# Optimization experiments

Hardware: AMD Instinct MI355X
Metric: run time of the kernel (lower is better)

Reference implementation:

```python
import jax, jax.numpy as jnp
import numpy as np

EMBED_DIM = 1024
HEAD_NUM = 16
HEAD_DIM = EMBED_DIM // HEAD_NUM
T, B, S = 2048, 4, 2048


def setup_inputs() -> dict:
    key = jax.random.key(0)
    ks = jax.random.split(key, 11)
    s = 0.02
    return {
        "query": jax.random.normal(ks[0], (T, B, EMBED_DIM), jnp.float32),
        "key": jax.random.normal(ks[1], (S, B, EMBED_DIM), jnp.float32),
        "value": jax.random.normal(ks[2], (S, B, EMBED_DIM), jnp.float32),
        "q_proj_weight": jax.random.normal(ks[3], (EMBED_DIM, EMBED_DIM), jnp.float32) * s,
        "k_proj_weight": jax.random.normal(ks[4], (EMBED_DIM, EMBED_DIM), jnp.float32) * s,
        "v_proj_weight": jax.random.normal(ks[5], (EMBED_DIM, EMBED_DIM), jnp.float32) * s,
        "in_proj_bias": jax.random.normal(ks[6], (3 * EMBED_DIM,), jnp.float32) * s,
        "bias_k": jax.random.normal(ks[7], (1, 1, EMBED_DIM), jnp.float32) * s,
        "bias_v": jax.random.normal(ks[8], (1, 1, EMBED_DIM), jnp.float32) * s,
        "out_proj_weight": jax.random.normal(ks[9], (EMBED_DIM, EMBED_DIM), jnp.float32) * s,
        "out_proj_bias": jax.random.normal(ks[10], (EMBED_DIM,), jnp.float32) * s,
    }


def reference(query, key, value, q_proj_weight, k_proj_weight, v_proj_weight,
              in_proj_bias, bias_k, bias_v, out_proj_weight, out_proj_bias):
    t, b, e = query.shape
    h, hd = HEAD_NUM, HEAD_DIM
    scaling = float(hd) ** -0.5
    # input projections (F.linear: x @ W.T + b)
    q = (query @ q_proj_weight.T + in_proj_bias[:e]) * scaling          # [T,B,E]
    k = key @ k_proj_weight.T + in_proj_bias[e:2 * e]                   # [S,B,E]
    v = value @ v_proj_weight.T + in_proj_bias[2 * e:]                  # [S,B,E]
    # append bias_k / bias_v token along the sequence dim
    k = jnp.concatenate([k, jnp.broadcast_to(bias_k, (1, b, e))], axis=0)  # [S+1,B,E]
    v = jnp.concatenate([v, jnp.broadcast_to(bias_v, (1, b, e))], axis=0)  # [S+1,B,E]
    # split heads: [L, B, E] -> [B*H, L, hd]
    q = q.reshape(t, b * h, hd).transpose(1, 0, 2)
    k = k.reshape(-1, b * h, hd).transpose(1, 0, 2)
    v = v.reshape(-1, b * h, hd).transpose(1, 0, 2)
    # full O(T*S) attention, as in the original bmm->softmax->bmm
    weights = jax.nn.softmax(jnp.einsum('nqd,nkd->nqk', q, k), axis=-1)  # [B*H,T,S+1]
    out = jnp.einsum('nqk,nkd->nqd', weights, v)                         # [B*H,T,hd]
    out = out.transpose(1, 0, 2).reshape(t, b, e)
    out = out @ out_proj_weight.T + out_proj_bias
    avg_weights = weights.sum(axis=1) / h                                # [B*H,S+1]
    return out, avg_weights
```

## Files before the change

kernel.cpp:

```cpp
#include <hip/hip_runtime.h>

#define T_DIM 2048
#define B_DIM 4
#define S_DIM 2048
#define E_DIM 1024
#define H_NUM 16
#define HD    64
#define NH    64
#define SP1   2049
#define SPAD  2112
#define NCHUNK 33
#define NTOKE ((size_t)T_DIM * B_DIM * E_DIM)

typedef short bf16x8 __attribute__((ext_vector_type(8)));
typedef short bf16x4 __attribute__((ext_vector_type(4)));
typedef float f32x4  __attribute__((ext_vector_type(4)));
typedef float f32x16 __attribute__((ext_vector_type(16)));
typedef unsigned int u32;

#define QSCALE 0.18033688011112042f

#if __has_builtin(__builtin_amdgcn_exp2f)
__device__ __forceinline__ float exp2_fast(float x) { return __builtin_amdgcn_exp2f(x); }
#else
__device__ __forceinline__ float exp2_fast(float x) { return __expf(x * 0.6931471805599453f); }
#endif

__device__ __forceinline__ unsigned short f2bf(float x) {
    union { float f; unsigned int u; } v; v.f = x;
    unsigned int r = v.u + 0x7FFFu + ((v.u >> 16) & 1u);
    return (unsigned short)(r >> 16);
}

__device__ __forceinline__ u32 cvtpk_bf16(float lo, float hi) {
    u32 r;
    asm("v_cvt_pk_bf16_f32 %0, %1, %2" : "=v"(r) : "v"(lo), "v"(hi));
    return r;
}
__device__ __forceinline__ void plswap(u32& a, u32& b) {
    asm("v_permlane32_swap_b32 %0, %1" : "+v"(a), "+v"(b));
}

__device__ __forceinline__ void load_lds16(const void* g, void* l) {
    __builtin_amdgcn_global_load_lds(
        (const __attribute__((address_space(1))) unsigned int*)g,
        (__attribute__((address_space(3))) unsigned int*)l, 16, 0, 0);
}

__global__ __launch_bounds__(256)
void cvt_w4(const float* __restrict__ w0, const float* __restrict__ w1,
            const float* __restrict__ w2, const float* __restrict__ w3,
            short* __restrict__ dst)
{
    const int y = blockIdx.y;
    const float* src = (y == 0) ? w0 : (y == 1) ? w1 : (y == 2) ? w2 : w3;
    short* d = dst + (size_t)y * E_DIM * E_DIM;
    const int i = blockIdx.x * 256 + threadIdx.x;
    const float4* s = reinterpret_cast<const float4*>(src) + (size_t)i * 2;
    float4 a = s[0], b = s[1];
    uint4 o;
    o.x = cvtpk_bf16(a.x, a.y); o.y = cvtpk_bf16(a.z, a.w);
    o.z = cvtpk_bf16(b.x, b.y); o.w = cvtpk_bf16(b.z, b.w);
    *(reinterpret_cast<uint4*>(d) + i) = o;
}

__global__ __launch_bounds__(256)
void cvt_in(const float* __restrict__ q, const float* __restrict__ k,
            const float* __restrict__ v, short* __restrict__ dst)
{
    const int y = blockIdx.y;
    const float* src = (y == 0) ? q : (y == 1) ? k : v;
    short* d = dst + (size_t)y * NTOKE;
    const size_t i = (size_t)blockIdx.x * 256 + threadIdx.x;
    const float4* s = reinterpret_cast<const float4*>(src) + i * 2;
    float4 a = s[0], b = s[1];
    uint4 o;
    o.x = cvtpk_bf16(a.x, a.y); o.y = cvtpk_bf16(a.z, a.w);
    o.z = cvtpk_bf16(b.x, b.y); o.w = cvtpk_bf16(b.z, b.w);
    *(reinterpret_cast<uint4*>(d) + i) = o;
}

template<int MODE>
__global__ __launch_bounds__(256, 4)
void gemm_bf16(const short* __restrict__ Abase, const short* __restrict__ Wall,
               const float* __restrict__ biasAll, void* __restrict__ outp)
{
    __shared__ short As[128][64];
    __shared__ short Bs[128][64];
    const int bm = blockIdx.x, bn = blockIdx.y;
    const int z = (MODE == 0) ? blockIdx.z : 0;
    const short* Az = Abase + (MODE == 0 ? (size_t)z * NTOKE : 0);
    const short* W  = Wall + (size_t)z * E_DIM * E_DIM;
    const float* bias = biasAll + z * E_DIM;

    const int tid = threadIdx.x;
    const int l = tid & 63, w = tid >> 6;
    const int wr = w >> 1, wc = w & 1;
    const int lr = l & 15, lg = l >> 4;
    const int srow = tid >> 3, scol = (tid & 7) * 8;

    f32x4 acc[4][4] = {};

    for (int k0 = 0; k0 < E_DIM; k0 += 64) {
#pragma unroll
        for (int r = 0; r < 4; ++r) {
            const int row = r * 32 + srow;
            const short* ga;
            if (MODE == 3) {
                const int m = bm * 128 + row;
                ga = Az + ((size_t)((m & 3) * 16 + (k0 >> 6)) * T_DIM + (m >> 2)) * HD + scol;
            } else {
                ga = Az + (size_t)(bm * 128 + row) * E_DIM + k0 + scol;
            }
            load_lds16(ga, &As[row][scol]);
            load_lds16(W + (size_t)(bn * 128 + row) * E_DIM + k0 + scol, &Bs[row][scol]);
        }
        __syncthreads();

        __builtin_amdgcn_s_setprio(1);
#pragma unroll
        for (int c = 0; c < 2; ++c) {
            bf16x8 af[4], bf[4];
#pragma unroll
            for (int mi = 0; mi < 4; ++mi)
                af[mi] = *reinterpret_cast<const bf16x8*>(&As[wr * 64 + mi * 16 + lr][c * 32 + lg * 8]);
#pragma unroll
            for (int ni = 0; ni < 4; ++ni)
                bf[ni] = *reinterpret_cast<const bf16x8*>(&Bs[wc * 64 + ni * 16 + lr][c * 32 + lg * 8]);
#pragma unroll
            for (int mi = 0; mi < 4; ++mi)
#pragma unroll
                for (int ni = 0; ni < 4; ++ni)
                    acc[mi][ni] = __builtin_amdgcn_mfma_f32_16x16x32_bf16(
                        af[mi], bf[ni], acc[mi][ni], 0, 0, 0);
        }
        __builtin_amdgcn_s_setprio(0);
        __syncthreads();
    }

#pragma unroll
    for (int mi = 0; mi < 4; ++mi)
#pragma unroll
        for (int ni = 0; ni < 4; ++ni) {
            const int colg = bn * 128 + wc * 64 + ni * 16 + lr;
            const float bv = bias[colg];
#pragma unroll
            for (int r = 0; r < 4; ++r) {
                const int m = bm * 128 + wr * 64 + mi * 16 + lg * 4 + r;
                float v = acc[mi][ni][r] + bv;
                if (MODE == 3) {
                    ((float*)outp)[(size_t)m * E_DIM + colg] = v;
                } else {
                    if (z == 0) v *= QSCALE;
                    const int seq = m >> 2, b = m & 3;
                    const int head = colg >> 6, d = colg & 63;
                    const int sd = (z == 0) ? T_DIM : SPAD;
                    short* ob = (short*)outp;
                    if (z == 1) ob += (size_t)NH * T_DIM * HD;
                    else if (z == 2) ob += (size_t)NH * T_DIM * HD + (size_t)NH * SPAD * HD;
                    ob[((size_t)(b * 16 + head) * sd + seq) * HD + d] = (short)f2bf(v);
                }
            }
        }
}

__global__ void fill_kv_pad(short* __restrict__ k_h, short* __restrict__ v_h,
                            const float* __restrict__ bias_k,
                            const float* __restrict__ bias_v)
{
    const int d   = threadIdx.x;
    const int row = S_DIM + blockIdx.x;
    const int n   = blockIdx.y;
    short bk = 0, bv = 0;
    if (row == S_DIM) {
        bk = (short)f2bf(bias_k[(n & 15) * HD + d]);
        bv = (short)f2bf(bias_v[(n & 15) * HD + d]);
    }
    const size_t idx = ((size_t)n * SPAD + row) * HD + d;
    k_h[idx] = bk;
    v_h[idx] = bv;
}

__global__ __launch_bounds__(512, 4)
void attn_mfma(const short* __restrict__ q_h, const short* __restrict__ k_h,
               const short* __restrict__ v_h, short* __restrict__ o_h,
               float* __restrict__ m_arr, float* __restrict__ l_arr)
{
    __shared__ short KsD[2][64 * 64];
    __shared__ short VtD[2][64 * 64];

    const int id = blockIdx.x;
    const int xcd = id & 7, slot = id >> 3;
    const int n = xcd * 8 + (slot >> 3);
    const int q0 = (slot & 7) * 256;

    const int tid = threadIdx.x, l = tid & 63, w = tid >> 6;
    const int ql = l & 31;
    const int hi = l >> 5;
    const int qrow = q0 + w * 32 + ql;

    const int krow = tid >> 3, kcg = tid & 7;
    const int kswz = (kcg * 16) ^ ((krow & 7) << 4);
    const int sp = tid & 31, dq = tid >> 5;

    const short* kbase = k_h + (size_t)n * SPAD * HD;
    const short* vbase = v_h + (size_t)n * SPAD * HD;

    bf16x8 aq0, aq1, aq2, aq3;
    {
        const short* qp = q_h + ((size_t)n * T_DIM + qrow) * HD + hi * 8;
        aq0 = *(const bf16x8*)(qp);
        aq1 = *(const bf16x8*)(qp + 16);
        aq2 = *(const bf16x8*)(qp + 32);
        aq3 = *(const bf16x8*)(qp + 48);
    }

    bf16x8 pk  = *(const bf16x8*)(kbase + (size_t)krow * HD + kcg * 8);
    bf16x4 pva = *(const bf16x4*)(vbase + (size_t)(2 * sp) * HD + dq * 4);
    bf16x4 pvb = *(const bf16x4*)(vbase + (size_t)(2 * sp + 1) * HD + dq * 4);
    {
        char* KsB = (char*)KsD[0];
        char* VtB = (char*)VtD[0];
        *(bf16x8*)(KsB + krow * 128 + kswz) = pk;
#pragma unroll
        for (int j = 0; j < 4; ++j) {
            u32 pkd = (u32)(unsigned short)pva[j] | ((u32)(unsigned short)pvb[j] << 16);
            const int d = dq * 4 + j;
            *(u32*)(VtB + d * 128 + ((4 * sp) ^ ((d & 7) << 4))) = pkd;
        }
    }
    __syncthreads();

    float m_run = -1e30f, l_run = 0.f;
    f32x16 accA, accB;
#pragma unroll
    for (int r = 0; r < 16; ++r) { accA[r] = 0.f; accB[r] = 0.f; }

    for (int kc = 0; kc < NCHUNK; ++kc) {
        const char* KsB = (const char*)KsD[kc & 1];
        const char* VtB = (const char*)VtD[kc & 1];
        const bool more = (kc + 1 < NCHUNK);

        if (more) {
            const int s0n = (kc + 1) * 64;
            pk  = *(const bf16x8*)(kbase + (size_t)(s0n + krow) * HD + kcg * 8);
            pva = *(const bf16x4*)(vbase + (size_t)(s0n + 2 * sp) * HD + dq * 4);
            pvb = *(const bf16x4*)(vbase + (size_t)(s0n + 2 * sp + 1) * HD + dq * 4);
        }

        f32x16 sc0, sc1;
#pragma unroll
        for (int r = 0; r < 16; ++r) { sc0[r] = 0.f; sc1[r] = 0.f; }
        __builtin_amdgcn_s_setprio(1);
#pragma unroll
        for (int sl = 0; sl < 4; ++sl) {
            const int cb = ((sl * 32) + hi * 16) ^ ((ql & 7) << 4);
            bf16x8 kf0 = *(const bf16x8*)(KsB + ql * 128 + cb);
            bf16x8 kf1 = *(const bf16x8*)(KsB + (32 + ql) * 128 + cb);
            bf16x8 qf = (sl == 0) ? aq0 : (sl == 1) ? aq1 : (sl == 2) ? aq2 : aq3;
            sc0 = __builtin_amdgcn_mfma_f32_32x32x16_bf16(kf0, qf, sc0, 0, 0, 0);
            sc1 = __builtin_amdgcn_mfma_f32_32x32x16_bf16(kf1, qf, sc1, 0, 0, 0);
        }
        __builtin_amdgcn_s_setprio(0);

        const int s0 = kc * 64;
        if (s0 + 64 > SP1) {
#pragma unroll
            for (int r = 0; r < 16; ++r) {
                const int key = (r & 3) + 8 * (r >> 2) + 4 * hi;
                if (s0 + key >= SP1)      sc0[r] = -1e30f;
                if (s0 + 32 + key >= SP1) sc1[r] = -1e30f;
            }
        }

        float mv[16];
#pragma unroll
        for (int r = 0; r < 16; ++r) mv[r] = fmaxf(sc0[r], sc1[r]);
#pragma unroll
        for (int s = 8; s > 0; s >>= 1)
#pragma unroll
            for (int r = 0; r < s; ++r) mv[r] = fmaxf(mv[r], mv[r + s]);
        float mx = fmaxf(mv[0], __shfl_xor(mv[0], 32));
        if (!__all(mx - m_run <= 8.0f)) {
            const float mnew = fmaxf(m_run, mx);
            const float fac = exp2_fast(m_run - mnew);
            l_run *= fac;
#pragma unroll
            for (int r = 0; r < 16; ++r) { accA[r] *= fac; accB[r] *= fac; }
            m_run = mnew;
        }
        float p0[16], p1[16];
#pragma unroll
        for (int r = 0; r < 16; ++r) p0[r] = exp2_fast(sc0[r] - m_run);
#pragma unroll
        for (int r = 0; r < 16; ++r) p1[r] = exp2_fast(sc1[r] - m_run);
        float sv[16];
#pragma unroll
        for (int r = 0; r < 16; ++r) sv[r] = p0[r] + p1[r];
#pragma unroll
        for (int s = 8; s > 0; s >>= 1)
#pragma unroll
            for (int r = 0; r < s; ++r) sv[r] += sv[r + s];
        l_run += sv[0] + __shfl_xor(sv[0], 32);

        union PF { u32 u[4]; bf16x8 v; };
        PF pf0, pf1, pf2, pf3;
        {
            u32 a0 = cvtpk_bf16(p0[0], p0[1]),   b0 = cvtpk_bf16(p0[4], p0[5]);   plswap(a0, b0);
            u32 a1 = cvtpk_bf16(p0[2], p0[3]),   b1 = cvtpk_bf16(p0[6], p0[7]);   plswap(a1, b1);
            u32 a2 = cvtpk_bf16(p0[8], p0[9]),   b2 = cvtpk_bf16(p0[12], p0[13]); plswap(a2, b2);
            u32 a3 = cvtpk_bf16(p0[10], p0[11]), b3 = cvtpk_bf16(p0[14], p0[15]); plswap(a3, b3);
            pf0.u[0] = a0; pf0.u[1] = a1; pf0.u[2] = b0; pf0.u[3] = b1;
            pf1.u[0] = a2; pf1.u[1] = a3; pf1.u[2] = b2; pf1.u[3] = b3;
            u32 c0 = cvtpk_bf16(p1[0], p1[1]),   d0_ = cvtpk_bf16(p1[4], p1[5]);   plswap(c0, d0_);
            u32 c1 = cvtpk_bf16(p1[2], p1[3]),   d1_ = cvtpk_bf16(p1[6], p1[7]);   plswap(c1, d1_);
            u32 c2 = cvtpk_bf16(p1[8], p1[9]),   d2_ = cvtpk_bf16(p1[12], p1[13]); plswap(c2, d2_);
            u32 c3 = cvtpk_bf16(p1[10], p1[11]), d3_ = cvtpk_bf16(p1[14], p1[15]); plswap(c3, d3_);
            pf2.u[0] = c0; pf2.u[1] = c1; pf2.u[2] = d0_; pf2.u[3] = d1_;
            pf3.u[0] = c2; pf3.u[1] = c3; pf3.u[2] = d2_; pf3.u[3] = d3_;
        }

        __builtin_amdgcn_s_setprio(1);
#pragma unroll
        for (int ksl = 0; ksl < 4; ++ksl) {
            const int cb = ((ksl * 32) + hi * 16) ^ ((ql & 7) << 4);
            bf16x8 vf0 = *(const bf16x8*)(VtB + ql * 128 + cb);
            bf16x8 vf1 = *(const bf16x8*)(VtB + (32 + ql) * 128 + cb);
            const bf16x8 pv = (ksl == 0) ? pf0.v : (ksl == 1) ? pf1.v : (ksl == 2) ? pf2.v : pf3.v;
            accA = __builtin_amdgcn_mfma_f32_32x32x16_bf16(vf0, pv, accA, 0, 0, 0);
            accB = __builtin_amdgcn_mfma_f32_32x32x16_bf16(vf1, pv, accB, 0, 0, 0);
        }
        __builtin_amdgcn_s_setprio(0);

        if (more) {
            char* KsN = (char*)KsD[(kc & 1) ^ 1];
            char* VtN = (char*)VtD[(kc & 1) ^ 1];
            *(bf16x8*)(KsN + krow * 128 + kswz) = pk;
#pragma unroll
            for (int j = 0; j < 4; ++j) {
                u32 pkd = (u32)(unsigned short)pva[j] | ((u32)(unsigned short)pvb[j] << 16);
                const int d = dq * 4 + j;
                *(u32*)(VtN + d * 128 + ((4 * sp) ^ ((d & 7) << 4))) = pkd;
            }
            __syncthreads();
        }
    }

    const float il = 1.0f / l_run;
    short* orow = o_h + ((size_t)n * T_DIM + qrow) * HD;
#pragma unroll
    for (int rq = 0; rq < 4; ++rq) {
        uint2 st;
        st.x = cvtpk_bf16(accA[rq * 4 + 0] * il, accA[rq * 4 + 1] * il);
        st.y = cvtpk_bf16(accA[rq * 4 + 2] * il, accA[rq * 4 + 3] * il);
        *(uint2*)(orow + rq * 8 + hi * 4) = st;
        uint2 st2;
        st2.x = cvtpk_bf16(accB[rq * 4 + 0] * il, accB[rq * 4 + 1] * il);
        st2.y = cvtpk_bf16(accB[rq * 4 + 2] * il, accB[rq * 4 + 3] * il);
        *(uint2*)(orow + 32 + rq * 8 + hi * 4) = st2;
    }
    if (hi == 0) {
        m_arr[n * T_DIM + qrow] = m_run;
        l_arr[n * T_DIM + qrow] = l_run;
    }
}

__global__ __launch_bounds__(256)
void colsum_mfma(const short* __restrict__ q_h, const short* __restrict__ k_h,
                 const float* __restrict__ m_arr, const float* __restrict__ l_arr,
                 float* __restrict__ avg_out)
{
    __shared__ short Qs[2][64][72];
    __shared__ float msh[2][64];
    __shared__ float lih[2][64];

    const int id = blockIdx.x;
    const int xcd = id & 7, slot = id >> 3;
    const int n = xcd * 8 + slot / 33;
    const int s0 = (slot % 33) * 64;

    const int tid = threadIdx.x, l = tid & 63, w = tid >> 6;
    const int lr = l & 15, lg = l >> 4;
    const int qr = tid >> 3, qcg = tid & 7;

    const short* qbase = q_h + (size_t)n * T_DIM * HD;

    bf16x8 ak[2];
#pragma unroll
    for (int c = 0; c < 2; ++c)
        ak[c] = *reinterpret_cast<const bf16x8*>(
            k_h + ((size_t)n * SPAD + s0 + w * 16 + lr) * HD + c * 32 + lg * 8);

    bf16x8 qa = *(const bf16x8*)(qbase + (size_t)qr * HD + qcg * 8);
    bf16x8 qb = *(const bf16x8*)(qbase + (size_t)(32 + qr) * HD + qcg * 8);
    float mlv = 0.f;
    if (tid < 64) mlv = m_arr[n * T_DIM + tid];
    else if (tid < 128) mlv = l_arr[n * T_DIM + tid - 64];
    *(bf16x8*)&Qs[0][qr][qcg * 8] = qa;
    *(bf16x8*)&Qs[0][32 + qr][qcg * 8] = qb;
    if (tid < 64) msh[0][tid] = mlv;
    else if (tid < 128) lih[0][tid - 64] = 1.0f / mlv;
    __syncthreads();

    float csum[4] = {0.f, 0.f, 0.f, 0.f};

    for (int it = 0; it < T_DIM / 64; ++it) {
        const int buf = it & 1;
        const bool more = (it + 1 < T_DIM / 64);
        if (more) {
            const int qo = (it + 1) * 64;
            qa = *(const bf16x8*)(qbase + (size_t)(qo + qr) * HD + qcg * 8);
            qb = *(const bf16x8*)(qbase + (size_t)(qo + 32 + qr) * HD + qcg * 8);
            if (tid < 64) mlv = m_arr[n * T_DIM + qo + tid];
            else if (tid < 128) mlv = l_arr[n * T_DIM + qo + tid - 64];
        }
        __builtin_amdgcn_s_setprio(1);
#pragma unroll
        for (int qt = 0; qt < 4; ++qt) {
            bf16x8 bq0 = *reinterpret_cast<const bf16x8*>(&Qs[buf][qt * 16 + lr][lg * 8]);
            bf16x8 bq1 = *reinterpret_cast<const bf16x8*>(&Qs[buf][qt * 16 + lr][32 + lg * 8]);
            f32x4 z = {0.f, 0.f, 0.f, 0.f};
            z = __builtin_amdgcn_mfma_f32_16x16x32_bf16(ak[0], bq0, z, 0, 0, 0);
            z = __builtin_amdgcn_mfma_f32_16x16x32_bf16(ak[1], bq1, z, 0, 0, 0);
            const float mq = msh[buf][qt * 16 + lr];
            const float lq = lih[buf][qt * 16 + lr];
#pragma unroll
            for (int r = 0; r < 4; ++r)
                csum[r] += exp2_fast(z[r] - mq) * lq;
        }
        __builtin_amdgcn_s_setprio(0);
        if (more) {
            *(bf16x8*)&Qs[buf ^ 1][qr][qcg * 8] = qa;
            *(bf16x8*)&Qs[buf ^ 1][32 + qr][qcg * 8] = qb;
            if (tid < 64) msh[buf ^ 1][tid] = mlv;
            else if (tid < 128) lih[buf ^ 1][tid - 64] = 1.0f / mlv;
            __syncthreads();
        }
    }

#pragma unroll
    for (int r = 0; r < 4; ++r) {
        float v = csum[r];
        v += __shfl_xor(v, 1, 16);
        v += __shfl_xor(v, 2, 16);
        v += __shfl_xor(v, 4, 16);
        v += __shfl_xor(v, 8, 16);
        if (lr == 0) {
            const int key = s0 + w * 16 + lg * 4 + r;
            if (key < SP1) avg_out[(size_t)n * SP1 + key] = v * 0.0625f;
        }
    }
}

extern "C" void kernel_launch(void* const* d_in, const int* in_sizes, int n_in,
                              void* d_out, int out_size, void* d_ws, size_t ws_size,
                              hipStream_t stream)
{
    const float* query   = (const float*)d_in[0];
    const float* key     = (const float*)d_in[1];
    const float* value   = (const float*)d_in[2];
    const float* wq      = (const float*)d_in[3];
    const float* wk      = (const float*)d_in[4];
    const float* wv      = (const float*)d_in[5];
    const float* in_bias = (const float*)d_in[6];
    const float* bias_k  = (const float*)d_in[7];
    const float* bias_v  = (const float*)d_in[8];
    const float* wo      = (const float*)d_in[9];
    const float* out_b   = (const float*)d_in[10];
    float* out = (float*)d_out;

    short* wqb    = (short*)d_ws;
    short* wob    = wqb + (size_t)3 * E_DIM * E_DIM;
    short* qkv_bf = wqb + (size_t)4 * E_DIM * E_DIM;
    short* q_h = qkv_bf + 3 * NTOKE;
    short* k_h = q_h + (size_t)NH * T_DIM * HD;
    short* v_h = k_h + (size_t)NH * SPAD * HD;
    short* o_h = v_h + (size_t)NH * SPAD * HD;
    float* m_arr = (float*)(o_h + (size_t)NH * T_DIM * HD);
    float* l_arr = m_arr + (size_t)NH * T_DIM;

    const dim3 blk(256);
    hipLaunchKernelGGL(cvt_w4, dim3(512, 4), blk, 0, stream, wq, wk, wv, wo, wqb);
    hipLaunchKernelGGL(cvt_in, dim3(4096, 3), blk, 0, stream, query, key, value, qkv_bf);

    hipLaunchKernelGGL((gemm_bf16<0>), dim3(64, 8, 3), blk, 0, stream,
                       qkv_bf, wqb, in_bias, (void*)q_h);
    hipLaunchKernelGGL(fill_kv_pad, dim3(SPAD - S_DIM, NH), dim3(64), 0, stream,
                       k_h, v_h, bias_k, bias_v);
    hipLaunchKernelGGL(attn_mfma, dim3(512), dim3(512), 0, stream,
                       q_h, k_h, v_h, o_h, m_arr, l_arr);
    hipLaunchKernelGGL(colsum_mfma, dim3(2112), blk, 0, stream,
                       q_h, k_h, m_arr, l_arr, out + (size_t)T_DIM * B_DIM * E_DIM);
    hipLaunchKernelGGL((gemm_bf16<3>), dim3(64, 8), blk, 0, stream,
                       o_h, wob, out_b, (void*)out);
}
```

Baseline: 289.5 us.

## Fold max subtraction into MFMA init and compute row sums via ones-MFMA

Merges the two fp32-to-bf16 conversion kernels into one launch. In attention, the score accumulator now starts at -m_run, so the max subtraction rides in the MFMA and the per-element subtract goes away. The row-sum reduction is replaced by an extra MFMA against a ones vector, so the sum is taken over the bf16-rounded probabilities. The colsum kernel also seeds its MFMA with -m, and the rescale path shifts scores in place. This trades VALU and shuffle work for extra matrix instructions and slightly different rounding of the normaliser.

```diff
diff --git a/kernel.cpp b/kernel.cpp
--- a/kernel.cpp
+++ b/kernel.cpp
@@ -48,36 +48,38 @@
 }
 
 __global__ __launch_bounds__(256)
-void cvt_w4(const float* __restrict__ w0, const float* __restrict__ w1,
-            const float* __restrict__ w2, const float* __restrict__ w3,
-            short* __restrict__ dst)
+void cvt_all(const float* __restrict__ q, const float* __restrict__ k,
+             const float* __restrict__ v, const float* __restrict__ w0,
+             const float* __restrict__ w1, const float* __restrict__ w2,
+             const float* __restrict__ w3, short* __restrict__ indst,
+             short* __restrict__ wdst)
 {
     const int y = blockIdx.y;
-    const float* src = (y == 0) ? w0 : (y == 1) ? w1 : (y == 2) ? w2 : w3;
-    short* d = dst + (size_t)y * E_DIM * E_DIM;
-    const int i = blockIdx.x * 256 + threadIdx.x;
-    const float4* s = reinterpret_cast<const float4*>(src) + (size_t)i * 2;
-    float4 a = s[0], b = s[1];
-    uint4 o;
-    o.x = cvtpk_bf16(a.x, a.y); o.y = cvtpk_bf16(a.z, a.w);
-    o.z = cvtpk_bf16(b.x, b.y); o.w = cvtpk_bf16(b.z, b.w);
-    *(reinterpret_cast<uint4*>(d) + i) = o;
-}
-
-__global__ __launch_bounds__(256)
-void cvt_in(const float* __restrict__ q, const float* __restrict__ k,
-            const float* __restrict__ v, short* __restrict__ dst)
-{
-    const int y = blockIdx.y;
-    const float* src = (y == 0) ? q : (y == 1) ? k : v;
-    short* d = dst + (size_t)y * NTOKE;
-    const size_t i = (size_t)blockIdx.x * 256 + threadIdx.x;
-    const float4* s = reinterpret_cast<const float4*>(src) + i * 2;
-    float4 a = s[0], b = s[1];
-    uint4 o;
-    o.x = cvtpk_bf16(a.x, a.y); o.y = cvtpk_bf16(a.z, a.w);
-    o.z = cvtpk_bf16(b.x, b.y); o.w = cvtpk_bf16(b.z, b.w);
-    *(reinterpret_cast<uint4*>(d) + i) = o;
+    if (y < 3) {
+        const float* src = (y == 0) ? q : (y == 1) ? k : v;
+        short* d = indst + (size_t)y * NTOKE;
+        const size_t i = (size_t)blockIdx.x * 256 + threadIdx.x;
+        const float4* s = reinterpret_cast<const float4*>(src) + i * 2;
+        float4 a = s[0], b = s[1];
+        uint4 o;
+        o.x = cvtpk_bf16(a.x, a.y); o.y = cvtpk_bf16(a.z, a.w);
+        o.z = cvtpk_bf16(b.x, b.y); o.w = cvtpk_bf16(b.z, b.w);
+        *(reinterpret_cast<uint4*>(d) + i) = o;
+    } else {
+        const size_t gi = (size_t)blockIdx.x * 256 + threadIdx.x;
+        const size_t per = (size_t)E_DIM * E_DIM / 8;
+        if (gi >= 4 * per) return;
+        const int wsel = (int)(gi / per);
+        const size_t i = gi % per;
+        const float* src = (wsel == 0) ? w0 : (wsel == 1) ? w1 : (wsel == 2) ? w2 : w3;
+        short* d = wdst + (size_t)wsel * E_DIM * E_DIM;
+        const float4* s = reinterpret_cast<const float4*>(src) + i * 2;
+        float4 a = s[0], b = s[1];
+        uint4 o;
+        o.x = cvtpk_bf16(a.x, a.y); o.y = cvtpk_bf16(a.z, a.w);
+        o.z = cvtpk_bf16(b.x, b.y); o.w = cvtpk_bf16(b.z, b.w);
+        *(reinterpret_cast<uint4*>(d) + i) = o;
+    }
 }
 
 template<int MODE>
@@ -215,6 +217,10 @@
         aq3 = *(const bf16x8*)(qp + 48);
     }
 
+    bf16x8 onesf;
+#pragma unroll
+    for (int j = 0; j < 8; ++j) onesf[j] = (short)0x3F80;
+
     bf16x8 pk  = *(const bf16x8*)(kbase + (size_t)krow * HD + kcg * 8);
     bf16x4 pva = *(const bf16x4*)(vbase + (size_t)(2 * sp) * HD + dq * 4);
     bf16x4 pvb = *(const bf16x4*)(vbase + (size_t)(2 * sp + 1) * HD + dq * 4);
@@ -231,10 +237,10 @@
     }
     __syncthreads();
 
-    float m_run = -1e30f, l_run = 0.f;
-    f32x16 accA, accB;
-#pragma unroll
-    for (int r = 0; r < 16; ++r) { accA[r] = 0.f; accB[r] = 0.f; }
+    float m_run = 0.0f;
+    f32x16 accA, accB, accL;
+#pragma unroll
+    for (int r = 0; r < 16; ++r) { accA[r] = 0.f; accB[r] = 0.f; accL[r] = 0.f; }
 
     for (int kc = 0; kc < NCHUNK; ++kc) {
         const char* KsB = (const char*)KsD[kc & 1];
@@ -249,8 +255,9 @@
         }
 
         f32x16 sc0, sc1;
-#pragma unroll
-        for (int r = 0; r < 16; ++r) { sc0[r] = 0.f; sc1[r] = 0.f; }
+        const float nm = -m_run;
+#pragma unroll
+        for (int r = 0; r < 16; ++r) { sc0[r] = nm; sc1[r] = nm; }
         __builtin_amdgcn_s_setprio(1);
 #pragma unroll
         for (int sl = 0; sl < 4; ++sl) {
@@ -280,28 +287,22 @@
         for (int s = 8; s > 0; s >>= 1)
 #pragma unroll
             for (int r = 0; r < s; ++r) mv[r] = fmaxf(mv[r], mv[r + s]);
-        float mx = fmaxf(mv[0], __shfl_xor(mv[0], 32));
-        if (!__all(mx - m_run <= 8.0f)) {
-            const float mnew = fmaxf(m_run, mx);
-            const float fac = exp2_fast(m_run - mnew);
-            l_run *= fac;
-#pragma unroll
-            for (int r = 0; r < 16; ++r) { accA[r] *= fac; accB[r] *= fac; }
-            m_run = mnew;
+        const float mx = fmaxf(mv[0], __shfl_xor(mv[0], 32));
+        if (!__all(mx <= 8.0f)) {
+            const float sh = fmaxf(mx, 0.0f);
+            const float fac = exp2_fast(-sh);
+#pragma unroll
+            for (int r = 0; r < 16; ++r) {
+                accA[r] *= fac; accB[r] *= fac; accL[r] *= fac;
+                sc0[r] -= sh;   sc1[r] -= sh;
+            }
+            m_run += sh;
         }
         float p0[16], p1[16];
 #pragma unroll
-        for (int r = 0; r < 16; ++r) p0[r] = exp2_fast(sc0[r] - m_run);
-#pragma unroll
-        for (int r = 0; r < 16; ++r) p1[r] = exp2_fast(sc1[r] - m_run);
-        float sv[16];
-#pragma unroll
-        for (int r = 0; r < 16; ++r) sv[r] = p0[r] + p1[r];
-#pragma unroll
-        for (int s = 8; s > 0; s >>= 1)
-#pragma unroll
-            for (int r = 0; r < s; ++r) sv[r] += sv[r + s];
-        l_run += sv[0] + __shfl_xor(sv[0], 32);
+        for (int r = 0; r < 16; ++r) p0[r] = exp2_fast(sc0[r]);
+#pragma unroll
+        for (int r = 0; r < 16; ++r) p1[r] = exp2_fast(sc1[r]);
 
         union PF { u32 u[4]; bf16x8 v; };
         PF pf0, pf1, pf2, pf3;
@@ -329,6 +330,7 @@
             const bf16x8 pv = (ksl == 0) ? pf0.v : (ksl == 1) ? pf1.v : (ksl == 2) ? pf2.v : pf3.v;
             accA = __builtin_amdgcn_mfma_f32_32x32x16_bf16(vf0, pv, accA, 0, 0, 0);
             accB = __builtin_amdgcn_mfma_f32_32x32x16_bf16(vf1, pv, accB, 0, 0, 0);
+            accL = __builtin_amdgcn_mfma_f32_32x32x16_bf16(onesf, pv, accL, 0, 0, 0);
         }
         __builtin_amdgcn_s_setprio(0);
 
@@ -346,6 +348,7 @@
         }
     }
 
+    const float l_run = accL[0];
     const float il = 1.0f / l_run;
     short* orow = o_h + ((size_t)n * T_DIM + qrow) * HD;
 #pragma unroll
@@ -419,14 +422,16 @@
         for (int qt = 0; qt < 4; ++qt) {
             bf16x8 bq0 = *reinterpret_cast<const bf16x8*>(&Qs[buf][qt * 16 + lr][lg * 8]);
             bf16x8 bq1 = *reinterpret_cast<const bf16x8*>(&Qs[buf][qt * 16 + lr][32 + lg * 8]);
-            f32x4 z = {0.f, 0.f, 0.f, 0.f};
+            const float mq = msh[buf][qt * 16 + lr];
+            const float lq = lih[buf][qt * 16 + lr];
+            f32x4 z;
+#pragma unroll
+            for (int r = 0; r < 4; ++r) z[r] = -mq;
             z = __builtin_amdgcn_mfma_f32_16x16x32_bf16(ak[0], bq0, z, 0, 0, 0);
             z = __builtin_amdgcn_mfma_f32_16x16x32_bf16(ak[1], bq1, z, 0, 0, 0);
-            const float mq = msh[buf][qt * 16 + lr];
-            const float lq = lih[buf][qt * 16 + lr];
 #pragma unroll
             for (int r = 0; r < 4; ++r)
-                csum[r] += exp2_fast(z[r] - mq) * lq;
+                csum[r] += exp2_fast(z[r]) * lq;
         }
         __builtin_amdgcn_s_setprio(0);
         if (more) {
@@ -480,8 +485,8 @@
     float* l_arr = m_arr + (size_t)NH * T_DIM;
 
     const dim3 blk(256);
-    hipLaunchKernelGGL(cvt_w4, dim3(512, 4), blk, 0, stream, wq, wk, wv, wo, wqb);
-    hipLaunchKernelGGL(cvt_in, dim3(4096, 3), blk, 0, stream, query, key, value, qkv_bf);
+    hipLaunchKernelGGL(cvt_all, dim3(4096, 4), blk, 0, stream,
+                       query, key, value, wq, wk, wv, wo, qkv_bf, wqb);
 
     hipLaunchKernelGGL((gemm_bf16<0>), dim3(64, 8, 3), blk, 0, stream,
                        qkv_bf, wqb, in_bias, (void*)q_h);
```

Result: slower. 300.4 us (+3.8%).
